# Kernel optimization log

Measured on AMD Instinct MI355X. Metric: run time of the kernel, lower is better.

Reference implementation:

```python
import jax, jax.numpy as jnp
import numpy as np
from jax import lax

HEAD_DIM = 32
SCALE = HEAD_DIM ** -0.5
BN_EPS = 1e-5


def _bn_relu(x, g, b):
    # training-mode BatchNorm2d over (B,H,W) per channel, biased variance, then ReLU
    mean = jnp.mean(x, axis=(0, 1, 2))
    var = jnp.var(x, axis=(0, 1, 2))
    y = (x - mean) * lax.rsqrt(var + BN_EPS) * g + b
    return jax.nn.relu(y)


def _pool2x2(y, op):
    # AvgPool2d/MaxPool2d(kernel=2, stride=2) on [B,pH,pW,C]
    B, pH, pW, C = y.shape
    y = y.reshape(B, pH // 2, 2, pW // 2, 2, C)
    return op(y, axis=(2, 4))


def setup_inputs() -> dict:
    key = jax.random.key(0)
    ks = jax.random.split(key, 12)
    B, H, W, C, pC = 16, 32, 32, 512, 256
    s = lambda k, shape, fan: jax.random.normal(k, shape, jnp.float32) * (fan ** -0.5)
    return {
        "x": jax.random.normal(ks[0], (B, H, W, C), jnp.float32),
        "prevx": jax.random.normal(ks[1], (B, 2 * H, 2 * W, pC), jnp.float32),
        "w_prev_qkv": s(ks[2], (C, pC), pC),          # Linear(prev_dim->dim), no bias
        "w_qkv": s(ks[3], (C, C), C),                  # Linear(dim->dim), no bias
        "fuse_w": s(ks[4], (2 * C, C), 2 * C),         # 1x1 conv as [Cin, Cout]
        "fuse_b": jax.random.normal(ks[5], (C,), jnp.float32) * 0.01,
        "bn1_g": jnp.ones((C,), jnp.float32) + jax.random.normal(ks[6], (C,), jnp.float32) * 0.01,
        "bn1_b": jax.random.normal(ks[7], (C,), jnp.float32) * 0.01,
        "out_w": s(ks[8], (3, 3, C, C), 9 * C),        # 3x3 conv HWIO
        "out_b": jax.random.normal(ks[9], (C,), jnp.float32) * 0.01,
        "bn2_g": jnp.ones((C,), jnp.float32) + jax.random.normal(ks[10], (C,), jnp.float32) * 0.01,
        "bn2_b": jax.random.normal(ks[11], (C,), jnp.float32) * 0.01,
        "gamma": jnp.array([0.3], jnp.float32),
        "beta": jnp.array([0.4], jnp.float32),
    }


def reference(x, prevx, w_prev_qkv, w_qkv, fuse_w, fuse_b, bn1_g, bn1_b,
              out_w, out_b, bn2_g, bn2_b, gamma, beta):
    B, H, W, C = x.shape
    N = H * W

    prevqkv = prevx @ w_prev_qkv.T                       # [B,2H,2W,C]
    qkv = (x @ w_qkv.T).reshape(B, N, C)                 # [B,N,C]
    avg_kv = _pool2x2(prevqkv, jnp.mean).reshape(B, -1, C)
    max_kv = _pool2x2(prevqkv, jnp.max).reshape(B, -1, C)

    def attn(q, k, v):
        a = jax.nn.softmax(jnp.einsum('bnc,bmc->bnm', q, k) * SCALE, axis=-1)
        o = jnp.einsum('bnm,bmc->bnc', a, v)
        # faithful to torch: (attn@v).transpose(1,2).reshape(B,H,W,-1)
        return jnp.swapaxes(o, 1, 2).reshape(B, H, W, C)

    x_now = attn(qkv, qkv, qkv)
    avgx_prev = attn(qkv, avg_kv, avg_kv)
    maxx_prev = attn(qkv, max_kv, max_kv)
    x_prev = beta[0] * avgx_prev + (1.0 - beta[0]) * maxx_prev

    cat = jnp.concatenate([x_now, x_prev], axis=-1)      # [B,H,W,2C]
    fusx = _bn_relu(jnp.einsum('bhwi,io->bhwo', cat, fuse_w) + fuse_b, bn1_g, bn1_b)
    x = x + gamma[0] * fusx

    y = lax.conv_general_dilated(x, out_w, window_strides=(1, 1), padding='SAME',
                                 dimension_numbers=('NHWC', 'HWIO', 'NHWC')) + out_b
    return _bn_relu(y, bn2_g, bn2_b)
```

## Files before the change

kernel.cpp:

```cpp
#include <hip/hip_runtime.h>
#include <hip/hip_bf16.h>

#define B_   16
#define C_   512
#define N_   1024
#define NTOK 16384
#define SCALE_ 0.17677669529663687f
#define EPS_ 1e-5f

typedef __attribute__((ext_vector_type(8))) short bf16x8;
typedef __attribute__((ext_vector_type(4))) float f32x4;
typedef __attribute__((ext_vector_type(4))) short sh4;

#define GLOBAL_AS __attribute__((address_space(1)))
#define LDS_AS    __attribute__((address_space(3)))
#define MFMA16 __builtin_amdgcn_mfma_f32_16x16x32_bf16

__device__ __forceinline__ short f2bs(float v){
    __hip_bfloat16 h = __float2bfloat16(v);
    return *reinterpret_cast<short*>(&h);
}
__device__ __forceinline__ float bs2f(short s){
    __hip_bfloat16 h = *reinterpret_cast<__hip_bfloat16*>(&s);
    return __bfloat162float(h);
}
__device__ __forceinline__ void gload16(const void* g, void* l){
    __builtin_amdgcn_global_load_lds((const GLOBAL_AS unsigned int*)g,
                                     (LDS_AS unsigned int*)l, 16, 0, 0);
}

enum { AG_ROW = 0, AG_POOL = 1, AG_FUSE = 2, AG_CONV = 3, AG_SEL3 = 4 };
enum { EP_QKV = 0, EP_POOL = 1, EP_PVN = 7, EP_FUSE_STATS = 8, EP_SPLIT_F32 = 9 };
enum { ORD_INNER_N = 0, ORD_INNER_M = 1 };

__global__ __launch_bounds__(256) void k_zero(float* p, int n){
    int i = blockIdx.x*256 + threadIdx.x;
    if (i < n) p[i] = 0.f;
}

__global__ __launch_bounds__(256) void k_cast(const float* __restrict__ s, short* __restrict__ d, int n){
    int i = (blockIdx.x*256 + threadIdx.x)*4;
    if (i >= n) return;
    float4 v = *reinterpret_cast<const float4*>(s + i);
    sh4 o; o[0]=f2bs(v.x); o[1]=f2bs(v.y); o[2]=f2bs(v.z); o[3]=f2bs(v.w);
    *reinterpret_cast<sh4*>(d + i) = o;
}

__global__ __launch_bounds__(256) void k_tcast(const float* __restrict__ src, short* __restrict__ dst,
                                               int R, int Cc){
    __shared__ float t[32][33];
    int bx = blockIdx.x*32, by = blockIdx.y*32;
    int tx = threadIdx.x & 31, ty = threadIdx.x >> 5;
    #pragma unroll
    for (int i = 0; i < 32; i += 8)
        t[ty+i][tx] = src[(size_t)(by+ty+i)*Cc + bx+tx];
    __syncthreads();
    #pragma unroll
    for (int i = 0; i < 32; i += 8)
        dst[(size_t)(bx+ty+i)*R + by+tx] = f2bs(t[tx][ty+i]);
}

template<int AM, int EP, int ORDER, int NX, int NY, int NZ, int NT, int KT, int KROW, int KSPLIT,
         long ASTR, long BSTR>
__global__ __launch_bounds__(256) void k_mm(const short* __restrict__ A,
                                            const short* __restrict__ Bt,
                                            const short* __restrict__ A2,
                                            const float* __restrict__ sc0,
                                            void* __restrict__ O0,
                                            void* __restrict__ O1,
                                            void* __restrict__ O2,
                                            void* __restrict__ O3){
    __shared__ short Asm[128*32];
    __shared__ short Bsm[128*32];
    const int tid = threadIdx.x, wave = tid >> 6, lane = tid & 63;

    constexpr int nwg = NX*NY*NZ;
    constexpr int q8 = nwg >> 3, r8 = nwg & 7;
    int orig = blockIdx.x;
    int xcd = orig & 7, idx8 = orig >> 3;
    int wg = (xcd < r8 ? xcd*(q8+1) : r8*(q8+1) + (xcd - r8)*q8) + idx8;
    int bz = wg / (NX*NY);
    int rem = wg - bz*(NX*NY);
    int nx, my;
    if constexpr (ORDER == ORD_INNER_N){ my = rem / NX; nx = rem - my*NX; }
    else                               { nx = rem / NY; my = rem - nx*NY; }

    const int m0 = my*128, n0 = nx*128;
    const short* Ab;
    if constexpr (AM == AG_SEL3){
        const short* base = (bz < 16) ? A : (bz < 32) ? A2 : (const short*)O3;
        Ab = base + (size_t)(bz & 15)*ASTR;
    } else {
        Ab = A + (size_t)bz*ASTR;
    }
    const short* Bb = Bt + (size_t)bz*BSTR;

    f32x4 acc[4][4];
    #pragma unroll
    for (int i = 0; i < 4; ++i)
        #pragma unroll
        for (int j = 0; j < 4; ++j)
            acc[i][j] = (f32x4){0.f,0.f,0.f,0.f};

    const int wm = (wave >> 1)*64, wn = (wave & 1)*64;
    const int lrow = lane & 15, lk = (lane >> 4)*8;

    for (int k0 = 0; k0 < KT; k0 += 32){
        #pragma unroll
        for (int is = 0; is < 2; ++is){
            int fl = is*256 + tid;
            int r = fl >> 2, ccol = (fl & 3)*8;
            int kk = bz*KSPLIT + k0 + ccol;
            const short* ga;
            if constexpr (AM == AG_ROW || AM == AG_SEL3){
                ga = Ab + (size_t)(m0 + r)*KROW + kk;
            } else if constexpr (AM == AG_POOL){
                int m = m0 + r;
                int b = m >> 12, rem2 = m & 4095, g = rem2 >> 2, qd = rem2 & 3;
                int srow = (b*64 + (g>>5)*2 + (qd>>1))*64 + (g&31)*2 + (qd&1);
                ga = Ab + (size_t)srow*KROW + kk;
            } else if constexpr (AM == AG_FUSE){
                int m = m0 + r;
                int b = m >> 10, rem2 = m & 1023, h = rem2 >> 5, w = rem2 & 31;
                const short* src = (kk < 512) ? A : A2;
                ga = src + ((size_t)(b*512 + h*16 + (w>>1))*1024 + ((w&1)<<9) + (kk & 511));
            } else {
                int m = m0 + r;
                int b = m >> 10, rem2 = m & 1023, h = rem2 >> 5, w = rem2 & 31;
                int tap = kk >> 9, ic = kk & 511;
                int dh = tap/3 - 1, dw = tap - (tap/3)*3 - 1;
                int hs = h + dh, wd = w + dw;
                if (hs >= 0 && hs < 32 && wd >= 0 && wd < 32)
                    ga = A + ((size_t)((b*32 + hs)*32 + wd)*512 + ic);
                else
                    ga = A2;
            }
            gload16(ga, &Asm[(is*4 + wave)*512]);
            const short* gb = Bb + (size_t)(n0 + r)*KROW + kk;
            gload16(gb, &Bsm[(is*4 + wave)*512]);
        }
        __syncthreads();
        bf16x8 af[4], bfr[4];
        #pragma unroll
        for (int mi = 0; mi < 4; ++mi)
            af[mi] = *(const bf16x8*)&Asm[(wm + mi*16 + lrow)*32 + lk];
        #pragma unroll
        for (int nj = 0; nj < 4; ++nj)
            bfr[nj] = *(const bf16x8*)&Bsm[(wn + nj*16 + lrow)*32 + lk];
        #pragma unroll
        for (int mi = 0; mi < 4; ++mi)
            #pragma unroll
            for (int nj = 0; nj < 4; ++nj)
                acc[mi][nj] = MFMA16(af[mi], bfr[nj], acc[mi][nj], 0, 0, 0);
        __syncthreads();
    }

    const int lg = lane >> 4;

    if constexpr (EP == EP_FUSE_STATS){
        float* redS = (float*)Asm;
        float* redQ = (float*)Bsm;
        #pragma unroll
        for (int nj = 0; nj < 4; ++nj){
            int c = n0 + wn + nj*16 + lrow;
            float bias = sc0[c];
            float s = 0.f, qq = 0.f;
            #pragma unroll
            for (int mi = 0; mi < 4; ++mi){
                int r0 = m0 + wm + mi*16 + lg*4;
                #pragma unroll
                for (int rg = 0; rg < 4; ++rg){
                    float val = acc[mi][nj][rg] + bias;
                    s += val; qq += val*val;
                    ((short*)O0)[(size_t)(r0+rg)*NT + c] = f2bs(val);
                }
            }
            int chl = wn + nj*16 + lrow;
            int slot = (wave >> 1)*4 + lg;
            redS[chl*8 + slot] = s;
            redQ[chl*8 + slot] = qq;
        }
        __syncthreads();
        if (tid < 128){
            float S = 0.f, Q = 0.f;
            #pragma unroll
            for (int k = 0; k < 8; ++k){ S += redS[tid*8 + k]; Q += redQ[tid*8 + k]; }
            atomicAdd(&((float*)O1)[n0 + tid], S);
            atomicAdd(&((float*)O2)[n0 + tid], Q);
        }
        return;
    }

    #pragma unroll
    for (int mi = 0; mi < 4; ++mi)
        #pragma unroll
        for (int nj = 0; nj < 4; ++nj){
            int c  = n0 + wn + nj*16 + lrow;
            int r0 = m0 + wm + mi*16 + lg*4;
            f32x4 v = acc[mi][nj];
            if constexpr (EP == EP_QKV){
                sh4 t4;
                #pragma unroll
                for (int rg = 0; rg < 4; ++rg){
                    short s = f2bs(v[rg]);
                    ((short*)O0)[(size_t)(r0+rg)*NT + c] = s;
                    t4[rg] = s;
                }
                int b = r0 >> 10, t = r0 & 1023;
                *reinterpret_cast<sh4*>((short*)O1 + ((size_t)(b*512 + c))*1024 + t) = t4;
            } else if constexpr (EP == EP_POOL){
                float av = 0.25f*(v[0]+v[1]+v[2]+v[3]);
                float mx = fmaxf(fmaxf(v[0],v[1]), fmaxf(v[2],v[3]));
                int g = r0 >> 2;
                int b = g >> 10, t = g & 1023;
                ((short*)O0)[(size_t)g*512 + c] = f2bs(av);
                ((short*)O2)[(size_t)g*512 + c] = f2bs(mx);
                ((short*)O1)[((size_t)(b*512 + c))*1024 + t] = f2bs(av);
                ((short*)O3)[((size_t)(b*512 + c))*1024 + t] = f2bs(mx);
            } else if constexpr (EP == EP_PVN){
                short* Ob = ((bz < 16) ? (short*)O0 : (bz < 32) ? (short*)O1 : (short*)O2)
                            + (size_t)(bz & 15)*524288;
                float sc = sc0[(size_t)bz*1024 + c];
                #pragma unroll
                for (int rg = 0; rg < 4; ++rg)
                    Ob[(size_t)(r0+rg)*NT + c] = f2bs(v[rg]*sc);
            } else {
                float* O = (float*)O0 + (size_t)bz*((long)NTOK*NT);
                #pragma unroll
                for (int rg = 0; rg < 4; ++rg)
                    O[(size_t)(r0+rg)*NT + c] = v[rg];
            }
        }
}

__global__ __launch_bounds__(256) void k_scorep(
    const short* __restrict__ Q,
    const short* __restrict__ K0, const short* __restrict__ K1, const short* __restrict__ K2,
    short* __restrict__ P, float* __restrict__ linvp)
{
    __shared__ short Kls[32*512];
    __shared__ short Pls[4][16][40];

    const int tid = threadIdx.x, wave = tid >> 6, lane = tid & 63;
    const int lrow = lane & 15, hi = lane >> 4;

    int orig = blockIdx.x;
    int wg = (orig & 7)*96 + (orig >> 3);
    int a = wg >> 8, rem = wg & 255;
    int b = rem >> 4, qt = rem & 15;

    const short* Kb = (a == 0 ? K0 : a == 1 ? K1 : K2) + (size_t)b*524288;
    const short* Qb = Q + (size_t)b*524288;
    short* Pb = P + ((size_t)(a*16 + b) << 20);
    const int m0 = qt*64 + wave*16;

    bf16x8 q[16];
    #pragma unroll
    for (int ks = 0; ks < 16; ++ks)
        q[ks] = *(const bf16x8*)&Qb[(size_t)(m0 + lrow)*512 + ks*32 + hi*8];

    const int swk = (lrow & 7) << 4;
    float lsum[4] = {0.f,0.f,0.f,0.f};

    for (int kv = 0; kv < 1024; kv += 32){
        #pragma unroll
        for (int it = 0; it < 8; ++it){
            int r = it*4 + wave;
            gload16(Kb + (size_t)(kv + r)*512 + (size_t)((lane ^ (r & 7))*8), &Kls[r*512]);
        }
        __syncthreads();
        f32x4 s0 = {0.f,0.f,0.f,0.f}, s1 = {0.f,0.f,0.f,0.f};
        #pragma unroll
        for (int ks = 0; ks < 16; ++ks){
            bf16x8 b0 = *(const bf16x8*)&Kls[lrow*512      + (((ks*64 + hi*16) ^ swk) >> 1)];
            bf16x8 b1 = *(const bf16x8*)&Kls[(16+lrow)*512 + (((ks*64 + hi*16) ^ swk) >> 1)];
            s0 = MFMA16(q[ks], b0, s0, 0, 0, 0);
            s1 = MFMA16(q[ks], b1, s1, 0, 0, 0);
        }
        #pragma unroll
        for (int r = 0; r < 4; ++r){
            float p0 = __expf(fminf(s0[r]*SCALE_, 80.f));
            float p1 = __expf(fminf(s1[r]*SCALE_, 80.f));
            lsum[r] += p0 + p1;
            Pls[wave][hi*4 + r][lrow]      = f2bs(p0);
            Pls[wave][hi*4 + r][16 + lrow] = f2bs(p1);
        }
        bf16x8 pk = *(const bf16x8*)&Pls[wave][lane >> 2][(lane & 3)*8];
        *reinterpret_cast<bf16x8*>(&Pb[(size_t)(m0 + (lane >> 2))*1024 + kv + (lane & 3)*8]) = pk;
        __syncthreads();
    }

    #pragma unroll
    for (int r = 0; r < 4; ++r){
        float s = lsum[r];
        #pragma unroll
        for (int off = 1; off < 16; off <<= 1) s += __shfl_xor(s, off);
        if (lrow == 0)
            linvp[(size_t)(a*16 + b)*1024 + m0 + hi*4 + r] = 1.f/s;
    }
}

__global__ __launch_bounds__(256) void k_combine(const short* __restrict__ av,
                                                 const short* __restrict__ mx,
                                                 short* __restrict__ o,
                                                 const float* __restrict__ beta){
    int i = (blockIdx.x*256 + threadIdx.x)*8;
    float be = beta[0];
    bf16x8 va = *(const bf16x8*)&av[i];
    bf16x8 vm = *(const bf16x8*)&mx[i];
    bf16x8 vo;
    #pragma unroll
    for (int j = 0; j < 8; ++j)
        vo[j] = f2bs(be*bs2f(va[j]) + (1.f - be)*bs2f(vm[j]));
    *reinterpret_cast<bf16x8*>(&o[i]) = vo;
}

__global__ __launch_bounds__(256) void k_stats2(const float* __restrict__ p0,
                                                const float* __restrict__ p1,
                                                const float* __restrict__ bias,
                                                float* __restrict__ Y,
                                                float* __restrict__ sum, float* __restrict__ sumsq){
    int t = threadIdx.x, c0 = t*2, r0 = blockIdx.x*32;
    float b0 = bias[c0], b1 = bias[c0+1];
    float s0=0, s1=0, q0=0, q1=0;
    for (int r = 0; r < 32; ++r){
        size_t off = (size_t)(r0+r)*C_ + c0;
        float2 a = *reinterpret_cast<const float2*>(p0 + off);
        float2 b = *reinterpret_cast<const float2*>(p1 + off);
        float v0 = a.x + b.x + b0, v1 = a.y + b.y + b1;
        float2 ov; ov.x = v0; ov.y = v1;
        *reinterpret_cast<float2*>(Y + off) = ov;
        s0 += v0; q0 += v0*v0; s1 += v1; q1 += v1*v1;
    }
    atomicAdd(&sum[c0],   s0); atomicAdd(&sum[c0+1],   s1);
    atomicAdd(&sumsq[c0], q0); atomicAdd(&sumsq[c0+1], q1);
}

__global__ __launch_bounds__(256) void k_apply1(const short* __restrict__ fusxq,
                                                const float* __restrict__ x,
                                                const float* __restrict__ sum,
                                                const float* __restrict__ sumsq,
                                                const float* __restrict__ g,
                                                const float* __restrict__ bb,
                                                const float* __restrict__ gamma,
                                                short* __restrict__ x2q){
    int i4 = (blockIdx.x*256 + threadIdx.x)*4;
    int c = i4 & (C_-1);
    sh4 f = *reinterpret_cast<const sh4*>(fusxq + i4);
    float4 xv = *reinterpret_cast<const float4*>(x + i4);
    float gm = gamma[0];
    sh4 o;
    #pragma unroll
    for (int j = 0; j < 4; ++j){
        int cj = c + j;
        float mean = sum[cj]*(1.f/NTOK);
        float var  = sumsq[cj]*(1.f/NTOK) - mean*mean;
        float t = (bs2f(f[j]) - mean)*rsqrtf(var + EPS_)*g[cj] + bb[cj];
        float xj = (j==0) ? xv.x : (j==1) ? xv.y : (j==2) ? xv.z : xv.w;
        o[j] = f2bs(xj + gm*fmaxf(t, 0.f));
    }
    *reinterpret_cast<sh4*>(x2q + i4) = o;
}

__global__ __launch_bounds__(256) void k_apply2(float* __restrict__ Y,
                                                const float* __restrict__ sum,
                                                const float* __restrict__ sumsq,
                                                const float* __restrict__ g,
                                                const float* __restrict__ bb){
    int i4 = (blockIdx.x*256 + threadIdx.x)*4;
    int c = i4 & (C_-1);
    float4 v = *reinterpret_cast<float4*>(Y + i4);
    float o[4] = {v.x, v.y, v.z, v.w};
    #pragma unroll
    for (int j = 0; j < 4; ++j){
        int cj = c + j;
        float mean = sum[cj]*(1.f/NTOK);
        float var  = sumsq[cj]*(1.f/NTOK) - mean*mean;
        float t = (o[j] - mean)*rsqrtf(var + EPS_)*g[cj] + bb[cj];
        o[j] = fmaxf(t, 0.f);
    }
    float4 ov; ov.x = o[0]; ov.y = o[1]; ov.z = o[2]; ov.w = o[3];
    *reinterpret_cast<float4*>(Y + i4) = ov;
}

extern "C" void kernel_launch(void* const* d_in, const int* in_sizes, int n_in,
                              void* d_out, int out_size, void* d_ws, size_t ws_size,
                              hipStream_t stream){
    const float* x      = (const float*)d_in[0];
    const float* prevx  = (const float*)d_in[1];
    const float* w_prev = (const float*)d_in[2];
    const float* w_qkv  = (const float*)d_in[3];
    const float* fuse_w = (const float*)d_in[4];
    const float* fuse_b = (const float*)d_in[5];
    const float* bn1_g  = (const float*)d_in[6];
    const float* bn1_b  = (const float*)d_in[7];
    const float* out_w  = (const float*)d_in[8];
    const float* out_b  = (const float*)d_in[9];
    const float* bn2_g  = (const float*)d_in[10];
    const float* bn2_b  = (const float*)d_in[11];
    const float* gamma  = (const float*)d_in[12];
    const float* beta   = (const float*)d_in[13];
    float* out = (float*)d_out;

    char* ws8 = (char*)d_ws;
    short* pxq  = (short*)(ws8 + 0);
    short* xq   = (short*)(ws8 + 33554432);
    short* Pall = (short*)(ws8 + 0);
    float* cpart= (float*)(ws8 + 0);
    short* qkvT = (short*)(ws8 + 100663296);
    short* x2q  = (short*)(ws8 + 100663296);
    short* avgkT= (short*)(ws8 + 117440512);
    short* maxkT= (short*)(ws8 + 134217728);
    short* prevT= maxkT;
    short* nowT = (short*)(ws8 + 150994944);
    short* avgk = nowT;
    short* avgT = (short*)(ws8 + 167772160);
    short* maxk = avgT;
    short* maxT = (short*)(ws8 + 184549376);
    short* fusxq= (short*)(ws8 + 184549376);
    short* qkv  = (short*)(ws8 + 201326592);
    short* wqT  = (short*)(ws8 + 218103808);
    short* wpT  = (short*)(ws8 + 218628096);
    short* wfT  = (short*)(ws8 + 218890240);
    short* wcT  = (short*)(ws8 + 219938816);
    float* st   = (float*)(ws8 + 224657408);
    short* zpg  = (short*)(ws8 + 224665600);
    float* linv = (float*)(ws8 + 224666624);
    float *s1sum = st, *s1sq = st + 512, *s2sum = st + 1024, *s2sq = st + 1536;

    dim3 blk(256);
    k_zero<<<9, blk, 0, stream>>>(st, 2304);
    k_cast<<<8192, blk, 0, stream>>>(x, xq, 8388608);
    k_cast<<<256,  blk, 0, stream>>>(w_qkv, wqT, 262144);
    k_cast<<<128,  blk, 0, stream>>>(w_prev, wpT, 131072);
    k_tcast<<<dim3(16, 32),  blk, 0, stream>>>(fuse_w, wfT, 1024, 512);
    k_tcast<<<dim3(16, 144), blk, 0, stream>>>(out_w, wcT, 4608, 512);
    k_cast<<<16384, blk, 0, stream>>>(prevx, pxq, 16777216);

    k_mm<AG_ROW, EP_QKV, ORD_INNER_N, 4, 128, 1, 512, 512, 512, 0, 0L, 0L>
        <<<512, blk, 0, stream>>>(xq, wqT, nullptr, nullptr,
                                  qkv, qkvT, nullptr, nullptr);
    k_mm<AG_POOL, EP_POOL, ORD_INNER_N, 4, 512, 1, 512, 256, 256, 0, 0L, 0L>
        <<<2048, blk, 0, stream>>>(pxq, wpT, nullptr, nullptr,
                                   avgk, avgkT, maxk, maxkT);
    k_scorep<<<768, blk, 0, stream>>>(qkv, qkv, avgk, maxk, Pall, linv);
    k_mm<AG_SEL3, EP_PVN, ORD_INNER_M, 8, 4, 48, 1024, 1024, 1024, 0, 524288L, 1048576L>
        <<<1536, blk, 0, stream>>>(qkvT, Pall, avgkT, linv,
                                   nowT, avgT, maxT, maxkT);
    k_combine<<<4096, blk, 0, stream>>>(avgT, maxT, prevT, beta);
    k_mm<AG_FUSE, EP_FUSE_STATS, ORD_INNER_N, 4, 128, 1, 512, 1024, 1024, 0, 0L, 0L>
        <<<512, blk, 0, stream>>>(nowT, wfT, prevT, fuse_b,
                                  fusxq, s1sum, s1sq, nullptr);
    k_apply1<<<8192, blk, 0, stream>>>(fusxq, x, s1sum, s1sq, bn1_g, bn1_b, gamma, x2q);
    k_mm<AG_CONV, EP_SPLIT_F32, ORD_INNER_N, 4, 128, 2, 512, 2304, 4608, 2304, 0L, 0L>
        <<<1024, blk, 0, stream>>>(x2q, wcT, zpg, nullptr,
                                   cpart, nullptr, nullptr, nullptr);
    k_stats2<<<512, blk, 0, stream>>>(cpart, cpart + (size_t)NTOK*C_, out_b, out, s2sum, s2sq);
    k_apply2<<<8192, blk, 0, stream>>>(out, s2sum, s2sq, bn2_g, bn2_b);
}
```

Measured before the change: 473.5 us.

## Compute attention scores with generic tiled GEMM kernel and atomic row sums

Replaces the dedicated score kernel, which streamed 32-key tiles per 64-query block, with the generic 128x128 LDS-tiled MFMA GEMM. The exponentiation and bf16 store of P now happen in a new epilogue, and row sums are accumulated with atomics into a zeroed buffer. The PV kernel now takes the reciprocal of the sum itself. This aims for better operand reuse and occupancy in the QK^T stage, at the cost of an extra zeroing launch, atomic traffic, and scattered 2-byte P stores.

Result: no change. 474.4 us (+0.2%).

```diff
diff --git a/kernel.cpp b/kernel.cpp
--- a/kernel.cpp
+++ b/kernel.cpp
@@ -29,8 +29,8 @@
                                      (LDS_AS unsigned int*)l, 16, 0, 0);
 }
 
-enum { AG_ROW = 0, AG_POOL = 1, AG_FUSE = 2, AG_CONV = 3, AG_SEL3 = 4 };
-enum { EP_QKV = 0, EP_POOL = 1, EP_PVN = 7, EP_FUSE_STATS = 8, EP_SPLIT_F32 = 9 };
+enum { AG_ROW = 0, AG_POOL = 1, AG_FUSE = 2, AG_CONV = 3, AG_SEL3 = 4, AG_QK = 5 };
+enum { EP_QKV = 0, EP_POOL = 1, EP_PVN = 7, EP_FUSE_STATS = 8, EP_SPLIT_F32 = 9, EP_SCOREP = 10 };
 enum { ORD_INNER_N = 0, ORD_INNER_M = 1 };
 
 __global__ __launch_bounds__(256) void k_zero(float* p, int n){
@@ -90,10 +90,18 @@
     if constexpr (AM == AG_SEL3){
         const short* base = (bz < 16) ? A : (bz < 32) ? A2 : (const short*)O3;
         Ab = base + (size_t)(bz & 15)*ASTR;
+    } else if constexpr (AM == AG_QK){
+        Ab = A + (size_t)(bz & 15)*ASTR;
     } else {
         Ab = A + (size_t)bz*ASTR;
     }
-    const short* Bb = Bt + (size_t)bz*BSTR;
+    const short* Bb;
+    if constexpr (AM == AG_QK){
+        const short* bbase = (bz < 16) ? Bt : (bz < 32) ? A2 : (const short*)O3;
+        Bb = bbase + (size_t)(bz & 15)*BSTR;
+    } else {
+        Bb = Bt + (size_t)bz*BSTR;
+    }
 
     f32x4 acc[4][4];
     #pragma unroll
@@ -112,7 +120,7 @@
             int r = fl >> 2, ccol = (fl & 3)*8;
             int kk = bz*KSPLIT + k0 + ccol;
             const short* ga;
-            if constexpr (AM == AG_ROW || AM == AG_SEL3){
+            if constexpr (AM == AG_ROW || AM == AG_SEL3 || AM == AG_QK){
                 ga = Ab + (size_t)(m0 + r)*KROW + kk;
             } else if constexpr (AM == AG_POOL){
                 int m = m0 + r;
@@ -191,6 +199,37 @@
         return;
     }
 
+    if constexpr (EP == EP_SCOREP){
+        short* Pb = (short*)O0 + ((size_t)bz << 20);
+        float* lsum = (float*)O1 + (size_t)bz*1024;
+        #pragma unroll
+        for (int mi = 0; mi < 4; ++mi){
+            int r0 = m0 + wm + mi*16 + lg*4;
+            float s4[4] = {0.f, 0.f, 0.f, 0.f};
+            #pragma unroll
+            for (int nj = 0; nj < 4; ++nj){
+                int c = n0 + wn + nj*16 + lrow;
+                f32x4 v = acc[mi][nj];
+                #pragma unroll
+                for (int rg = 0; rg < 4; ++rg){
+                    float p = __expf(fminf(v[rg]*SCALE_, 80.f));
+                    s4[rg] += p;
+                    Pb[(size_t)(r0+rg)*NT + c] = f2bs(p);
+                }
+            }
+            #pragma unroll
+            for (int off = 1; off < 16; off <<= 1){
+                #pragma unroll
+                for (int rg = 0; rg < 4; ++rg) s4[rg] += __shfl_xor(s4[rg], off);
+            }
+            if (lrow == 0){
+                #pragma unroll
+                for (int rg = 0; rg < 4; ++rg) atomicAdd(&lsum[r0+rg], s4[rg]);
+            }
+        }
+        return;
+    }
+
     #pragma unroll
     for (int mi = 0; mi < 4; ++mi)
         #pragma unroll
@@ -220,7 +259,7 @@
             } else if constexpr (EP == EP_PVN){
                 short* Ob = ((bz < 16) ? (short*)O0 : (bz < 32) ? (short*)O1 : (short*)O2)
                             + (size_t)(bz & 15)*524288;
-                float sc = sc0[(size_t)bz*1024 + c];
+                float sc = 1.f / sc0[(size_t)bz*1024 + c];
                 #pragma unroll
                 for (int rg = 0; rg < 4; ++rg)
                     Ob[(size_t)(r0+rg)*NT + c] = f2bs(v[rg]*sc);
@@ -231,73 +270,6 @@
                     O[(size_t)(r0+rg)*NT + c] = v[rg];
             }
         }
-}
-
-__global__ __launch_bounds__(256) void k_scorep(
-    const short* __restrict__ Q,
-    const short* __restrict__ K0, const short* __restrict__ K1, const short* __restrict__ K2,
-    short* __restrict__ P, float* __restrict__ linvp)
-{
-    __shared__ short Kls[32*512];
-    __shared__ short Pls[4][16][40];
-
-    const int tid = threadIdx.x, wave = tid >> 6, lane = tid & 63;
-    const int lrow = lane & 15, hi = lane >> 4;
-
-    int orig = blockIdx.x;
-    int wg = (orig & 7)*96 + (orig >> 3);
-    int a = wg >> 8, rem = wg & 255;
-    int b = rem >> 4, qt = rem & 15;
-
-    const short* Kb = (a == 0 ? K0 : a == 1 ? K1 : K2) + (size_t)b*524288;
-    const short* Qb = Q + (size_t)b*524288;
-    short* Pb = P + ((size_t)(a*16 + b) << 20);
-    const int m0 = qt*64 + wave*16;
-
-    bf16x8 q[16];
-    #pragma unroll
-    for (int ks = 0; ks < 16; ++ks)
-        q[ks] = *(const bf16x8*)&Qb[(size_t)(m0 + lrow)*512 + ks*32 + hi*8];
-
-    const int swk = (lrow & 7) << 4;
-    float lsum[4] = {0.f,0.f,0.f,0.f};
-
-    for (int kv = 0; kv < 1024; kv += 32){
-        #pragma unroll
-        for (int it = 0; it < 8; ++it){
-            int r = it*4 + wave;
-            gload16(Kb + (size_t)(kv + r)*512 + (size_t)((lane ^ (r & 7))*8), &Kls[r*512]);
-        }
-        __syncthreads();
-        f32x4 s0 = {0.f,0.f,0.f,0.f}, s1 = {0.f,0.f,0.f,0.f};
-        #pragma unroll
-        for (int ks = 0; ks < 16; ++ks){
-            bf16x8 b0 = *(const bf16x8*)&Kls[lrow*512      + (((ks*64 + hi*16) ^ swk) >> 1)];
-            bf16x8 b1 = *(const bf16x8*)&Kls[(16+lrow)*512 + (((ks*64 + hi*16) ^ swk) >> 1)];
-            s0 = MFMA16(q[ks], b0, s0, 0, 0, 0);
-            s1 = MFMA16(q[ks], b1, s1, 0, 0, 0);
-        }
-        #pragma unroll
-        for (int r = 0; r < 4; ++r){
-            float p0 = __expf(fminf(s0[r]*SCALE_, 80.f));
-            float p1 = __expf(fminf(s1[r]*SCALE_, 80.f));
-            lsum[r] += p0 + p1;
-            Pls[wave][hi*4 + r][lrow]      = f2bs(p0);
-            Pls[wave][hi*4 + r][16 + lrow] = f2bs(p1);
-        }
-        bf16x8 pk = *(const bf16x8*)&Pls[wave][lane >> 2][(lane & 3)*8];
-        *reinterpret_cast<bf16x8*>(&Pb[(size_t)(m0 + (lane >> 2))*1024 + kv + (lane & 3)*8]) = pk;
-        __syncthreads();
-    }
-
-    #pragma unroll
-    for (int r = 0; r < 4; ++r){
-        float s = lsum[r];
-        #pragma unroll
-        for (int off = 1; off < 16; off <<= 1) s += __shfl_xor(s, off);
-        if (lrow == 0)
-            linvp[(size_t)(a*16 + b)*1024 + m0 + hi*4 + r] = 1.f/s;
-    }
 }
 
 __global__ __launch_bounds__(256) void k_combine(const short* __restrict__ av,
@@ -425,11 +397,12 @@
     short* wcT  = (short*)(ws8 + 219938816);
     float* st   = (float*)(ws8 + 224657408);
     short* zpg  = (short*)(ws8 + 224665600);
-    float* linv = (float*)(ws8 + 224666624);
+    float* lsum = (float*)(ws8 + 224666624);
     float *s1sum = st, *s1sq = st + 512, *s2sum = st + 1024, *s2sq = st + 1536;
 
     dim3 blk(256);
     k_zero<<<9, blk, 0, stream>>>(st, 2304);
+    k_zero<<<192, blk, 0, stream>>>(lsum, 49152);
     k_cast<<<8192, blk, 0, stream>>>(x, xq, 8388608);
     k_cast<<<256,  blk, 0, stream>>>(w_qkv, wqT, 262144);
     k_cast<<<128,  blk, 0, stream>>>(w_prev, wpT, 131072);
@@ -443,9 +416,11 @@
     k_mm<AG_POOL, EP_POOL, ORD_INNER_N, 4, 512, 1, 512, 256, 256, 0, 0L, 0L>
         <<<2048, blk, 0, stream>>>(pxq, wpT, nullptr, nullptr,
                                    avgk, avgkT, maxk, maxkT);
-    k_scorep<<<768, blk, 0, stream>>>(qkv, qkv, avgk, maxk, Pall, linv);
+    k_mm<AG_QK, EP_SCOREP, ORD_INNER_M, 8, 8, 48, 1024, 512, 512, 0, 524288L, 524288L>
+        <<<3072, blk, 0, stream>>>(qkv, qkv, avgk, nullptr,
+                                   Pall, lsum, nullptr, maxk);
     k_mm<AG_SEL3, EP_PVN, ORD_INNER_M, 8, 4, 48, 1024, 1024, 1024, 0, 524288L, 1048576L>
-        <<<1536, blk, 0, stream>>>(qkvT, Pall, avgkT, linv,
+        <<<1536, blk, 0, stream>>>(qkvT, Pall, avgkT, lsum,
                                    nowT, avgT, maxT, maxkT);
     k_combine<<<4096, blk, 0, stream>>>(avgT, maxT, prevT, beta);
     k_mm<AG_FUSE, EP_FUSE_STATS, ORD_INNER_N, 4, 128, 1, 512, 1024, 1024, 0, 0L, 0L>
```
